# Kernel tuning notes

Hardware: AMD Instinct MI355X
Metric: run time of the kernel (lower is better)

Reference implementation:

```python
import jax, jax.numpy as jnp
import numpy as np

L, D, H, F = 6, 1024, 8, 2048
B, S, IN = 4, 2048, 128
DK = D // H
EPS = 1e-6


def layer_norm(x, s, b):
    mu = jnp.mean(x, -1, keepdims=True)
    var = jnp.mean((x - mu) ** 2, -1, keepdims=True)
    return (x - mu) * jax.lax.rsqrt(var + EPS) * s + b


def rotate_every_two(x):
    x1 = x[..., ::2]
    x2 = x[..., 1::2]
    return jnp.stack([-x2, x1], axis=-1).reshape(x.shape)


def rotary_tables():
    # torchscale RetNet xpos-style angles: each freq repeated twice (interleaved)
    angle = 1.0 / (10000.0 ** jnp.linspace(0.0, 1.0, DK // 2))
    angle = jnp.repeat(angle, 2)                      # [DK]
    idx = jnp.arange(S, dtype=jnp.float32)[:, None]   # [S,1]
    return jnp.sin(idx * angle), jnp.cos(idx * angle)  # [S,DK] each


def decay_mask():
    # gamma_h = 1 - 2^(-5-h); D[h,n,m] = gamma_h^(n-m) for n>=m else 0,
    # row-normalized by sqrt(row sum) as in torchscale.
    gamma = 1.0 - 2.0 ** (-5.0 - jnp.arange(H, dtype=jnp.float32))  # [H]
    n = jnp.arange(S)
    diff = jnp.clip(n[:, None] - n[None, :], 0)                      # [S,S]
    tril = n[:, None] >= n[None, :]
    m = jnp.where(tril[None], gamma[:, None, None] ** diff[None].astype(jnp.float32), 0.0)
    return m / jnp.sqrt(jnp.sum(m, -1, keepdims=True))               # [H,S,S]


def setup_inputs() -> dict:
    key = jax.random.key(0)
    ks = iter(jax.random.split(key, 24))
    p = lambda shape: jax.random.normal(next(ks), shape, jnp.float32) * 0.02
    return {
        "x": jax.random.normal(next(ks), (B, S, IN), jnp.float32),
        "W_in": p((IN, D)), "b_in": jnp.zeros((D,), jnp.float32),
        "Wq": p((L, D, D)), "Wk": p((L, D, D)), "Wv": p((L, D, D)),
        "Wg": p((L, D, D)), "Wo": p((L, D, D)),
        "gn_g": jnp.ones((L, D), jnp.float32),
        "ln1_s": jnp.ones((L, D), jnp.float32), "ln1_b": jnp.zeros((L, D), jnp.float32),
        "ffn_W1": p((L, D, F)), "ffn_b1": jnp.zeros((L, F), jnp.float32),
        "ffn_W2": p((L, F, D)), "ffn_b2": jnp.zeros((L, D), jnp.float32),
        "ln2_s": jnp.ones((L, D), jnp.float32), "ln2_b": jnp.zeros((L, D), jnp.float32),
        "lnf_s": jnp.ones((D,), jnp.float32), "lnf_b": jnp.zeros((D,), jnp.float32),
        "W_reg": p((D, 1)), "b_reg": jnp.zeros((1,), jnp.float32),
    }


def reference(x, W_in, b_in, Wq, Wk, Wv, Wg, Wo, gn_g, ln1_s, ln1_b,
              ffn_W1, ffn_b1, ffn_W2, ffn_b2, ln2_s, ln2_b, lnf_s, lnf_b,
              W_reg, b_reg):
    sin, cos = rotary_tables()
    dmask = decay_mask()  # [H,S,S]
    h = x @ W_in + b_in   # input_embed
    for l in range(L):
        # --- multi-scale retention (pre-norm) ---
        y = layer_norm(h, ln1_s[l], ln1_b[l])
        q = (y @ Wq[l]).reshape(B, S, H, DK).transpose(0, 2, 1, 3)
        k = (y @ Wk[l]).reshape(B, S, H, DK).transpose(0, 2, 1, 3) * (DK ** -0.5)
        v = (y @ Wv[l]).reshape(B, S, H, DK).transpose(0, 2, 1, 3)
        q = q * cos + rotate_every_two(q) * sin
        k = k * cos + rotate_every_two(k) * sin
        scores = jnp.einsum('bhnd,bhmd->bhnm', q, k)
        ret = scores * dmask[None]
        ret = ret / jnp.clip(jnp.abs(ret).sum(-1, keepdims=True), 1.0, None)
        o = jnp.einsum('bhnm,bhmd->bhnd', ret, v)
        # per-head group (RMS) norm
        o = o * jax.lax.rsqrt(jnp.mean(o * o, -1, keepdims=True) + EPS)
        o = o.transpose(0, 2, 1, 3).reshape(B, S, D) * gn_g[l]
        g = y @ Wg[l]
        h = h + (jax.nn.silu(g) * o) @ Wo[l]
        # --- FFN (pre-norm) ---
        y = layer_norm(h, ln2_s[l], ln2_b[l])
        h = h + jax.nn.gelu(y @ ffn_W1[l] + ffn_b1[l]) @ ffn_W2[l] + ffn_b2[l]
    h = layer_norm(h, lnf_s, lnf_b)
    out = 1.1 * jax.nn.sigmoid(h @ W_reg + b_reg) - 0.05
    return out.squeeze(-1)  # [B,S]
```

## Files before the change

### kernel.cpp

```cpp
#include <hip/hip_runtime.h>

#define L_ 6
#define D_ 1024
#define H_ 8
#define F_ 2048
#define B_ 4
#define S_ 2048
#define IN_ 128
#define DK_ 128
#define BS_ (B_*S_)
#define D2_ 4096

typedef short bf16x8 __attribute__((ext_vector_type(8)));
typedef float f32x4 __attribute__((ext_vector_type(4)));

__device__ inline float b2f(unsigned short u){ union{unsigned int i; float f;} v; v.i = ((unsigned int)u)<<16; return v.f; }
__device__ inline unsigned short f2b(float f){ union{unsigned int i; float f;} v; v.f = f; unsigned int r = v.i + 0x7FFFu + ((v.i>>16)&1u); return (unsigned short)(r>>16); }
__device__ inline unsigned int cvtpk(float lo, float hi){
    unsigned int r; asm("v_cvt_pk_bf16_f32 %0, %1, %2" : "=v"(r) : "v"(lo), "v"(hi)); return r;
}

__device__ inline void gld16(const void* g, void* l) {
    __builtin_amdgcn_global_load_lds((const __attribute__((address_space(1))) unsigned int*)g,
                                     (__attribute__((address_space(3))) unsigned int*)l, 16, 0, 0);
}

#define GBAR() do{ asm volatile("" ::: "memory"); __builtin_amdgcn_s_barrier(); asm volatile("" ::: "memory"); }while(0)

__global__ void f32_to_bf16_k(const float* __restrict__ in, unsigned short* __restrict__ out, int n)
{
    int i = blockIdx.x*256 + threadIdx.x;
    if (i < n) out[i] = f2b(in[i]);
}

__global__ void transpose_w_k(const float* __restrict__ in, unsigned short* __restrict__ out, int R, int C, size_t ostride)
{
    __shared__ float tile[32][33];
    int z = blockIdx.z;
    const float* pi = in + (size_t)z*R*C;
    unsigned short* po = out + (size_t)z*ostride;
    int c0 = blockIdx.x*32, r0 = blockIdx.y*32;
    int tx = threadIdx.x, ty = threadIdx.y;
    #pragma unroll
    for (int i=0;i<4;i++) tile[ty+i*8][tx] = pi[(size_t)(r0+ty+i*8)*C + c0+tx];
    __syncthreads();
    #pragma unroll
    for (int i=0;i<4;i++) po[(size_t)(c0+ty+i*8)*R + r0+tx] = f2b(tile[tx][ty+i*8]);
}

__global__ void transpose_v_k(const unsigned short* __restrict__ vb, unsigned short* __restrict__ vT)
{
    __shared__ unsigned short tile[32][33];
    int z = blockIdx.z;
    int b = z >> 3, hh = z & 7;
    int s0 = blockIdx.x*32, d0 = blockIdx.y*32;
    int tx = threadIdx.x, ty = threadIdx.y;
    #pragma unroll
    for (int i=0;i<4;i++) tile[ty+i*8][tx] = vb[(size_t)(b*S_ + s0+ty+i*8)*D2_ + hh*DK_ + d0+tx];
    __syncthreads();
    #pragma unroll
    for (int i=0;i<4;i++) vT[((size_t)z*DK_ + d0+ty+i*8)*S_ + s0+tx] = tile[tx][ty+i*8];
}

__global__ void build_sincos_k(float* __restrict__ cost, float* __restrict__ sint)
{
    int id = blockIdx.x*256 + threadIdx.x;
    int s = id >> 6, i = id & 63;
    float ang = powf(10000.f, -(float)i/63.f);
    float a = (float)s * ang;
    float sv = sinf(a), cv = cosf(a);
    sint[s*DK_ + 2*i] = sv; sint[s*DK_ + 2*i+1] = sv;
    cost[s*DK_ + 2*i] = cv; cost[s*DK_ + 2*i+1] = cv;
}

__global__ void build_dnorm_k(float* __restrict__ dnorm)
{
    int id = blockIdx.x*256 + threadIdx.x;
    int h = id >> 11, n = id & (S_-1);
    double g = 1.0 - exp2((double)(-5 - h));
    double sum = (1.0 - exp(((double)(n+1))*log(g))) / (1.0 - g);
    dnorm[id] = (float)(1.0/sqrt(sum));
}

__device__ inline float bsum(float v, float* red, int t)
{
    #pragma unroll
    for (int m=32; m; m>>=1) v += __shfl_xor(v, m);
    __syncthreads();
    if ((t & 63) == 0) red[t>>6] = v;
    __syncthreads();
    return red[0]+red[1]+red[2]+red[3];
}

__global__ __launch_bounds__(256) void ln_to_bf16_k(const float* __restrict__ x, const float* __restrict__ s,
                                                    const float* __restrict__ b, unsigned short* __restrict__ y)
{
    __shared__ float red[4];
    int row = blockIdx.x, t = threadIdx.x;
    const float* xr = x + (size_t)row * D_;
    float4 v = ((const float4*)xr)[t];
    float mu = bsum(v.x+v.y+v.z+v.w, red, t) * (1.f/D_);
    float d0=v.x-mu, d1=v.y-mu, d2=v.z-mu, d3=v.w-mu;
    float var = bsum(d0*d0+d1*d1+d2*d2+d3*d3, red, t) * (1.f/D_);
    float inv = rsqrtf(var + 1e-6f);
    int c = t*4;
    float o0 = d0*inv*s[c+0] + b[c+0];
    float o1 = d1*inv*s[c+1] + b[c+1];
    float o2 = d2*inv*s[c+2] + b[c+2];
    float o3 = d3*inv*s[c+3] + b[c+3];
    unsigned long long pk = (unsigned long long)f2b(o0) | ((unsigned long long)f2b(o1)<<16)
                          | ((unsigned long long)f2b(o2)<<32) | ((unsigned long long)f2b(o3)<<48);
    *(unsigned long long*)(y + (size_t)row*D_ + c) = pk;
}

template<int MODE, int BM, int BN, int WMC, int WNC>
__global__ __launch_bounds__(WMC*WNC*64, ((BM/WMC)*(BN/WNC) >= 128*64) ? 2 : 3)
void gemm4(const unsigned short* __restrict__ A,
           const unsigned short* __restrict__ Bt,
           const float* __restrict__ bias,
           void* __restrict__ Cv,
           int M, int N, int K)
{
    constexpr int THR = WMC*WNC*64;
    constexpr int IR  = BM/WMC/16;
    constexpr int JR  = BN/WNC/16;
    constexpr int ASZ = BM*64;
    constexpr int BSZ = BN*64;
    constexpr int RP  = THR/4;
    constexpr int AP  = BM/RP;
    constexpr int BP  = BN/RP;
    constexpr int Sa  = AP + BP;
    __shared__ unsigned char lds[2*(ASZ+BSZ)];

    const int tid = threadIdx.x, lane = tid & 63, w = tid >> 6;
    const int r16 = lane & 15, quad = (lane >> 4) & 3;
    const int wm = w / WNC, wn = w % WNC;

    const int nwg = (int)(gridDim.x * gridDim.y);
    int bid = (int)(blockIdx.y * gridDim.x + blockIdx.x);
    if ((nwg & 7) == 0) bid = (bid & 7) * (nwg >> 3) + (bid >> 3);
    const int m0 = (bid / (int)gridDim.x) * BM;
    const int n0 = (bid % (int)gridDim.x) * BN;

    const int srow = tid >> 2;
    const int schk = (tid & 3) ^ ((tid >> 3) & 3);
    const unsigned short* gA = A  + (size_t)(m0 + srow) * K + schk*8;
    const unsigned short* gB = Bt + (size_t)(n0 + srow) * K + schk*8;

    const int rchk = (quad ^ ((r16 >> 1) & 3)) * 16;
    const int aoff = (wm*(BM/WMC) + r16)*64 + rchk;
    const int boff = (wn*(BN/WNC) + r16)*64 + rchk;

    f32x4 acc[IR][JR];
    #pragma unroll
    for (int i=0;i<IR;i++)
      #pragma unroll
      for (int j=0;j<JR;j++) acc[i][j] = (f32x4){0.f,0.f,0.f,0.f};

    const int NT = K >> 5;

    auto stage = [&](int t){
        unsigned char* la = lds + (t&1)*(ASZ+BSZ);
        unsigned char* lb = la + ASZ;
        const size_t ko = (size_t)t * 32;
        #pragma unroll
        for (int p=0;p<AP;p++)
            gld16(gA + ko + (size_t)(p*RP)*K, la + p*RP*64 + tid*16);
        #pragma unroll
        for (int p=0;p<BP;p++)
            gld16(gB + ko + (size_t)(p*RP)*K, lb + p*RP*64 + tid*16);
    };

    auto compute = [&](int t){
        const unsigned char* ab = lds + (t&1)*(ASZ+BSZ);
        const unsigned char* bb = ab + ASZ;
        bf16x8 af[IR], bg[JR];
        #pragma unroll
        for (int i=0;i<IR;i++) af[i] = *(const bf16x8*)(ab + aoff + i*1024);
        #pragma unroll
        for (int j=0;j<JR;j++) bg[j] = *(const bf16x8*)(bb + boff + j*1024);
        __builtin_amdgcn_s_setprio(1);
        #pragma unroll
        for (int i=0;i<IR;i++)
          #pragma unroll
          for (int j=0;j<JR;j++)
            acc[i][j] = __builtin_amdgcn_mfma_f32_16x16x32_bf16(af[i], bg[j], acc[i][j], 0,0,0);
        __builtin_amdgcn_s_setprio(0);
    };

    stage(0);
    for (int t = 0; t < NT; ++t) {
        if (t + 1 < NT) {
            stage(t + 1);
            if constexpr (Sa == 4) asm volatile("s_waitcnt vmcnt(4)" ::: "memory");
            else                   asm volatile("s_waitcnt vmcnt(6)" ::: "memory");
        } else {
            asm volatile("s_waitcnt vmcnt(0)" ::: "memory");
        }
        GBAR();
        compute(t);
        GBAR();
    }

    float* Cf = (float*)Cv;
    unsigned short* Cb = (unsigned short*)Cv;
    #pragma unroll
    for (int j=0;j<JR;j++) {
      const int ccol = n0 + wn*(BN/WNC) + j*16 + r16;
      const float bv = bias ? bias[ccol] : 0.f;
      #pragma unroll
      for (int i=0;i<IR;i++) {
        #pragma unroll
        for (int r=0;r<4;r++) {
          const int crow = m0 + wm*(BM/WMC) + i*16 + quad*4 + r;
          float v = acc[i][j][r];
          if (MODE == 0) { Cf[(size_t)crow*N + ccol] = v + bv; }
          else if (MODE == 1) { Cf[(size_t)crow*N + ccol] += v + bv; }
          else if (MODE == 2) { Cb[(size_t)crow*N + ccol] = f2b(v); }
          else {
            v += bv;
            float t3 = tanhf(0.7978845608028654f*(v + 0.044715f*v*v*v));
            Cb[(size_t)crow*N + ccol] = f2b(0.5f*v*(1.f + t3));
          }
        }
      }
    }
}

__global__ __launch_bounds__(256) void rope_qk_k(unsigned short* __restrict__ qkvg,
                                                 const float* __restrict__ cost, const float* __restrict__ sint)
{
    int id = blockIdx.x*256 + threadIdx.x;
    int row = id >> 9;
    int d = (id & 511) * 2;
    int s = row & (S_-1);
    int dk = d & (DK_-1);
    float c0 = cost[s*DK_ + dk],   s0 = sint[s*DK_ + dk];
    float c1 = cost[s*DK_ + dk+1], s1 = sint[s*DK_ + dk+1];
    size_t off = (size_t)row*D2_ + d;
    unsigned int qu = *(unsigned int*)(qkvg + off);
    float q0 = b2f((unsigned short)(qu & 0xffffu)), q1 = b2f((unsigned short)(qu >> 16));
    float r0 = q0*c0 - q1*s0;
    float r1 = q1*c1 + q0*s1;
    *(unsigned int*)(qkvg + off) = (unsigned int)f2b(r0) | ((unsigned int)f2b(r1) << 16);
    const float sc = 0.08838834764831845f;
    unsigned int ku = *(unsigned int*)(qkvg + off + 1024);
    float k0 = b2f((unsigned short)(ku & 0xffffu))*sc, k1 = b2f((unsigned short)(ku >> 16))*sc;
    float t0 = k0*c0 - k1*s0;
    float t1 = k1*c1 + k0*s1;
    *(unsigned int*)(qkvg + off + 1024) = (unsigned int)f2b(t0) | ((unsigned int)f2b(t1) << 16);
}

__global__ __launch_bounds__(256, 2) void retention_k(const unsigned short* __restrict__ qk_base,
    const unsigned short* __restrict__ vT, const float* __restrict__ dnorm,
    const float* __restrict__ gng, unsigned short* __restrict__ attnin)
{
    __shared__ __align__(16) unsigned char lds[75776];
    const int pr = blockIdx.x;
    const int bh = blockIdx.y;
    const int b = bh >> 3, hh = bh & 7;
    const int tid = threadIdx.x, lane = tid & 63, w = tid >> 6;
    const int r16 = lane & 15, quad = lane >> 4;

    const float l2g = log2f(1.f - exp2f(-5.f - (float)hh));
    const int ithr = (int)(45.f / (-l2g));
    const unsigned int mkr = (r16 & 7) << 4;

    const int mk2  = ((tid >> 4) & 7) << 4;
    const int mkv2 = ((tid >> 3) & 7) << 4;
    const unsigned short* ksrc = qk_base + 1024 + ((size_t)(b*S_) + (tid>>4))*D2_ + hh*DK_
                                + ((((tid&15)*16) ^ mk2) >> 1);
    const unsigned short* vsrc = vT + ((size_t)bh*DK_ + (tid>>3))*S_ + ((((tid&7)*16) ^ mkv2) >> 1);

    float Aarr[4];
    #pragma unroll
    for (int r=0;r<4;r++) Aarr[r] = exp2f(l2g * (float)(63 - (w*16 + quad*4 + r)));

    float* dsums = (float*)(lds + 73728);
    float* ssums = (float*)(lds + 74752);

    auto stage = [&](int c2, int kt2){
        const unsigned short* s0 = ksrc + (size_t)kt2*64*D2_;
        #pragma unroll
        for (int i=0;i<4;i++)
            gld16(s0 + (size_t)i*16*D2_, lds + c2*16384 + i*4096 + w*1024);
        const unsigned short* s1 = vsrc + kt2*64;
        #pragma unroll
        for (int j=0;j<4;j++)
            gld16(s1 + (size_t)j*32*S_, lds + 32768 + c2*16384 + j*4096 + w*1024);
    };

    int cur = 0;

    #pragma unroll 1
    for (int seg = 0; seg < 2; ++seg) {
        const int qt = seg ? pr : (31 - pr);
        const int n0 = qt * 64;
        const int kt_start = max(0, (n0 - ithr) >> 6);

        bf16x8 qf[4][4];
        const unsigned short* qptr = qk_base + ((size_t)(b*S_ + n0 + r16))*D2_ + hh*DK_;
        #pragma unroll
        for (int qtl=0;qtl<4;qtl++)
          #pragma unroll
          for (int c=0;c<4;c++) qf[qtl][c] = *(const bf16x8*)(qptr + qtl*16*D2_ + c*32 + quad*8);

        f32x4 oacc[4][2];
        #pragma unroll
        for (int qtl=0;qtl<4;qtl++)
          #pragma unroll
          for (int dt=0;dt<2;dt++) oacc[qtl][dt] = (f32x4){0.f,0.f,0.f,0.f};
        float dsum[4] = {0.f,0.f,0.f,0.f};

        stage(cur, kt_start);

        #pragma unroll 1
        for (int kt = kt_start; kt <= qt; ++kt) {
            if (kt < qt) { stage(cur^1, kt+1); asm volatile("s_waitcnt vmcnt(8)" ::: "memory"); }
            else         { asm volatile("s_waitcnt vmcnt(0)" ::: "memory"); }
            GBAR();

            const unsigned char* kb = lds + cur*16384;
            bf16x8 kf[4];
            #pragma unroll
            for (int c=0;c<4;c++)
                kf[c] = *(const bf16x8*)(kb + (w*16 + r16)*256 + ((c*64 + quad*16) ^ mkr));
            f32x4 sf[4];
            #pragma unroll
            for (int qtl=0;qtl<4;qtl++) sf[qtl] = (f32x4){0.f,0.f,0.f,0.f};
            __builtin_amdgcn_s_setprio(1);
            #pragma unroll
            for (int c=0;c<4;c++)
              #pragma unroll
              for (int qtl=0;qtl<4;qtl++)
                sf[qtl] = __builtin_amdgcn_mfma_f32_16x16x32_bf16(kf[c], qf[qtl][c], sf[qtl], 0,0,0);
            __builtin_amdgcn_s_setprio(0);

            const bool diag = (kt == qt);
            #pragma unroll
            for (int qtl=0;qtl<4;qtl++) {
                float Bq = exp2f(l2g * (float)(n0 + qtl*16 + r16 - kt*64 - 63));
                float pv[4];
                #pragma unroll
                for (int r=0;r<4;r++) {
                    float p = sf[qtl][r] * Aarr[r] * Bq;
                    if (diag && (w*16 + quad*4 + r > qtl*16 + r16)) p = 0.f;
                    dsum[qtl] += fabsf(p);
                    pv[r] = p;
                }
                unsigned long long pk = (unsigned long long)cvtpk(pv[0], pv[1])
                                      | ((unsigned long long)cvtpk(pv[2], pv[3]) << 32);
                *(unsigned long long*)(lds + 65536 + (qtl*16 + r16)*128 + ((w*32 + quad*8) ^ mkr)) = pk;
            }
            asm volatile("s_waitcnt lgkmcnt(0)" ::: "memory");
            GBAR();

            const unsigned char* vb = lds + 32768 + cur*16384;
            bf16x8 pa[4][2], vf[2][2];
            #pragma unroll
            for (int qtl=0;qtl<4;qtl++)
              #pragma unroll
              for (int ks=0;ks<2;ks++)
                pa[qtl][ks] = *(const bf16x8*)(lds + 65536 + (qtl*16 + r16)*128 + ((ks*64 + quad*16) ^ mkr));
            #pragma unroll
            for (int dt=0;dt<2;dt++)
              #pragma unroll
              for (int ks=0;ks<2;ks++)
                vf[dt][ks] = *(const bf16x8*)(vb + (w*32 + dt*16 + r16)*128 + ((ks*64 + quad*16) ^ mkr));
            __builtin_amdgcn_s_setprio(1);
            #pragma unroll
            for (int qtl=0;qtl<4;qtl++)
              #pragma unroll
              for (int dt=0;dt<2;dt++)
                #pragma unroll
                for (int ks=0;ks<2;ks++)
                  oacc[qtl][dt] = __builtin_amdgcn_mfma_f32_16x16x32_bf16(pa[qtl][ks], vf[dt][ks], oacc[qtl][dt], 0,0,0);
            __builtin_amdgcn_s_setprio(0);
            GBAR();
            cur ^= 1;
        }

        #pragma unroll
        for (int qtl=0;qtl<4;qtl++) {
            float dv = dsum[qtl];
            dv += __shfl_xor(dv, 16); dv += __shfl_xor(dv, 32);
            if (lane < 16) dsums[w*64 + qtl*16 + r16] = dv;
        }
        __syncthreads();
        float scl[4][4], pss[4][4];
        #pragma unroll
        for (int qtl=0;qtl<4;qtl++) {
            #pragma unroll
            for (int r=0;r<4;r++) {
                int nl = qtl*16 + quad*4 + r;
                float dv = dsums[nl] + dsums[64+nl] + dsums[128+nl] + dsums[192+nl];
                float nr = dnorm[hh*S_ + n0 + nl];
                float sc = nr / fmaxf(1.f, dv * nr);
                scl[qtl][r] = sc;
                float s2 = 0.f;
                #pragma unroll
                for (int dt=0;dt<2;dt++) { float t = oacc[qtl][dt][r]*sc; s2 += t*t; }
                s2 += __shfl_xor(s2,1); s2 += __shfl_xor(s2,2);
                s2 += __shfl_xor(s2,4); s2 += __shfl_xor(s2,8);
                pss[qtl][r] = s2;
            }
        }
        if (r16 == 0) {
            #pragma unroll
            for (int qtl=0;qtl<4;qtl++)
              #pragma unroll
              for (int r=0;r<4;r++)
                ssums[w*64 + qtl*16 + quad*4 + r] = pss[qtl][r];
        }
        __syncthreads();
        #pragma unroll
        for (int qtl=0;qtl<4;qtl++) {
            float rms[4];
            #pragma unroll
            for (int r=0;r<4;r++) {
                int nl = qtl*16 + quad*4 + r;
                float s2 = ssums[nl] + ssums[64+nl] + ssums[128+nl] + ssums[192+nl];
                rms[r] = rsqrtf(s2*(1.f/DK_) + 1e-6f);
            }
            #pragma unroll
            for (int dt=0;dt<2;dt++) {
                int d = w*32 + dt*16 + r16;
                float gg = gng[hh*DK_ + d];
                #pragma unroll
                for (int r=0;r<4;r++) {
                    int n = n0 + qtl*16 + quad*4 + r;
                    float gv = b2f(qk_base[(size_t)(b*S_ + n)*D2_ + 3072 + hh*DK_ + d]);
                    float sg = gv / (1.f + expf(-gv));
                    float ov = oacc[qtl][dt][r]*scl[qtl][r]*rms[r]*gg;
                    attnin[(size_t)(b*S_ + n)*D_ + hh*DK_ + d] = f2b(ov*sg);
                }
            }
        }
        __syncthreads();
    }
}

__global__ __launch_bounds__(256) void head_out_k(const float* __restrict__ h, const float* __restrict__ s,
    const float* __restrict__ b, const float* __restrict__ wreg, const float* __restrict__ breg,
    float* __restrict__ out)
{
    __shared__ float red[4];
    int row = blockIdx.x, t = threadIdx.x;
    const float* xr = h + (size_t)row*D_;
    float4 v = ((const float4*)xr)[t];
    float mu = bsum(v.x+v.y+v.z+v.w, red, t) * (1.f/D_);
    float d0=v.x-mu, d1=v.y-mu, d2=v.z-mu, d3=v.w-mu;
    float var = bsum(d0*d0+d1*d1+d2*d2+d3*d3, red, t) * (1.f/D_);
    float inv = rsqrtf(var + 1e-6f);
    int c = t*4;
    float dot = (d0*inv*s[c+0]+b[c+0])*wreg[c+0] + (d1*inv*s[c+1]+b[c+1])*wreg[c+1]
              + (d2*inv*s[c+2]+b[c+2])*wreg[c+2] + (d3*inv*s[c+3]+b[c+3])*wreg[c+3];
    dot = bsum(dot, red, t);
    if (t == 0) out[row] = 1.1f / (1.f + expf(-(dot + breg[0]))) - 0.05f;
}

extern "C" void kernel_launch(void* const* d_in, const int* in_sizes, int n_in,
                              void* d_out, int out_size, void* d_ws, size_t ws_size,
                              hipStream_t stream)
{
    (void)in_sizes; (void)n_in; (void)out_size; (void)ws_size;
    const float* x    = (const float*)d_in[0];
    const float* W_in = (const float*)d_in[1];
    const float* b_in = (const float*)d_in[2];
    const float* Wq   = (const float*)d_in[3];
    const float* Wk   = (const float*)d_in[4];
    const float* Wv   = (const float*)d_in[5];
    const float* Wg   = (const float*)d_in[6];
    const float* Wo   = (const float*)d_in[7];
    const float* gn_g = (const float*)d_in[8];
    const float* ln1s = (const float*)d_in[9];
    const float* ln1b = (const float*)d_in[10];
    const float* W1   = (const float*)d_in[11];
    const float* b1   = (const float*)d_in[12];
    const float* W2   = (const float*)d_in[13];
    const float* b2   = (const float*)d_in[14];
    const float* ln2s = (const float*)d_in[15];
    const float* ln2b = (const float*)d_in[16];
    const float* lnfs = (const float*)d_in[17];
    const float* lnfb = (const float*)d_in[18];
    const float* Wreg = (const float*)d_in[19];
    const float* breg = (const float*)d_in[20];

    char* ws = (char*)d_ws;
    size_t off = 0;
    auto alloc = [&](size_t bytes) { char* p = ws + off; off += (bytes + 255) & ~(size_t)255; return p; };

    const size_t DD = (size_t)D_*D_;
    unsigned short* wqkvgT = (unsigned short*)alloc((size_t)L_*4*DD*2);
    unsigned short* woT  = (unsigned short*)alloc((size_t)L_*DD*2);
    unsigned short* w1T  = (unsigned short*)alloc((size_t)L_*D_*F_*2);
    unsigned short* w2T  = (unsigned short*)alloc((size_t)L_*D_*F_*2);
    unsigned short* winT = (unsigned short*)alloc((size_t)D_*IN_*2);
    unsigned short* x_bf = (unsigned short*)alloc((size_t)BS_*IN_*2);
    float*          hbuf = (float*)alloc((size_t)BS_*D_*4);
    unsigned short* y_bf = (unsigned short*)alloc((size_t)BS_*D_*2);
    unsigned short* qkvg = (unsigned short*)alloc((size_t)BS_*D2_*2);
    unsigned short* vTb  = (unsigned short*)alloc((size_t)BS_*D_*2);
    float*          cost = (float*)alloc((size_t)S_*DK_*4);
    float*          sint = (float*)alloc((size_t)S_*DK_*4);
    float*          dnrm = (float*)alloc((size_t)H_*S_*4);
    unsigned short* attn = y_bf;
    unsigned short* midb = qkvg;

    dim3 tb(32, 8);

    f32_to_bf16_k<<<(BS_*IN_)/256, 256, 0, stream>>>(x, x_bf, BS_*IN_);
    transpose_w_k<<<dim3(32,32,L_), tb, 0, stream>>>(Wq, wqkvgT + 0*DD, D_, D_, 4*DD);
    transpose_w_k<<<dim3(32,32,L_), tb, 0, stream>>>(Wk, wqkvgT + 1*DD, D_, D_, 4*DD);
    transpose_w_k<<<dim3(32,32,L_), tb, 0, stream>>>(Wv, wqkvgT + 2*DD, D_, D_, 4*DD);
    transpose_w_k<<<dim3(32,32,L_), tb, 0, stream>>>(Wg, wqkvgT + 3*DD, D_, D_, 4*DD);
    transpose_w_k<<<dim3(32,32,L_), tb, 0, stream>>>(Wo, woT, D_, D_, DD);
    transpose_w_k<<<dim3(64,32,L_), tb, 0, stream>>>(W1, w1T, D_, F_, (size_t)D_*F_);
    transpose_w_k<<<dim3(32,64,L_), tb, 0, stream>>>(W2, w2T, F_, D_, (size_t)D_*F_);
    transpose_w_k<<<dim3(32, 4, 1), tb, 0, stream>>>(W_in, winT, IN_, D_, (size_t)D_*IN_);
    build_sincos_k<<<(S_*64)/256, 256, 0, stream>>>(cost, sint);
    build_dnorm_k<<<(H_*S_)/256, 256, 0, stream>>>(dnrm);

    gemm4<0,128,128,2,2><<<dim3(D_/128, BS_/128), 256, 0, stream>>>(x_bf, winT, b_in, hbuf, BS_, D_, IN_);

    for (int l = 0; l < L_; ++l) {
        ln_to_bf16_k<<<BS_, 256, 0, stream>>>(hbuf, ln1s + l*D_, ln1b + l*D_, y_bf);
        gemm4<2,256,256,2,4><<<dim3(D2_/256, BS_/256), 512, 0, stream>>>(y_bf, wqkvgT + (size_t)l*4*DD, nullptr, qkvg, BS_, D2_, D_);
        rope_qk_k<<<(BS_*D_/2)/256, 256, 0, stream>>>(qkvg, cost, sint);
        transpose_v_k<<<dim3(S_/32, DK_/32, B_*H_), tb, 0, stream>>>(qkvg + 2048, vTb);
        retention_k<<<dim3(16, B_*H_), 256, 0, stream>>>(qkvg, vTb, dnrm, gn_g + l*D_, attn);
        gemm4<1,128,128,2,2><<<dim3(D_/128, BS_/128), 256, 0, stream>>>(attn, woT + (size_t)l*DD, nullptr, hbuf, BS_, D_, D_);
        ln_to_bf16_k<<<BS_, 256, 0, stream>>>(hbuf, ln2s + l*D_, ln2b + l*D_, y_bf);
        gemm4<3,256,128,2,2><<<dim3(F_/128, BS_/256), 256, 0, stream>>>(y_bf, w1T + (size_t)l*D_*F_, b1 + l*F_, midb, BS_, F_, D_);
        gemm4<1,128,128,2,2><<<dim3(D_/128, BS_/128), 256, 0, stream>>>(midb, w2T + (size_t)l*D_*F_, b2 + l*D_, hbuf, BS_, D_, F_);
    }

    head_out_k<<<BS_, 256, 0, stream>>>(hbuf, lnfs, lnfb, Wreg, breg, (float*)d_out);
}
```

Measured before the change: 2.144 ms.

## Replace GEMM with triple-buffered split-phase kernel using 256-wide N tiles

The templated GEMM becomes a fixed 512-thread, 8-wave kernel with BN=256 and BM of 128 or 256. Shared memory goes from double to triple buffering, with two K-steps prefetched ahead. Each K-step is split into two halves that interleave A and B stage loads with MFMA work. All projection and FFN GEMMs move to this kernel, so the Wo/W2/input GEMMs now use larger 128x256 tiles. The aim is to hide global-load latency and raise MFMA utilisation, at the cost of more LDS and barriers, fewer workgroups for the N=1024 GEMMs, and lower occupancy.

```diff
diff --git a/kernel.cpp b/kernel.cpp
--- a/kernel.cpp
+++ b/kernel.cpp
@@ -113,28 +113,27 @@
     *(unsigned long long*)(y + (size_t)row*D_ + c) = pk;
 }
 
-template<int MODE, int BM, int BN, int WMC, int WNC>
-__global__ __launch_bounds__(WMC*WNC*64, ((BM/WMC)*(BN/WNC) >= 128*64) ? 2 : 3)
-void gemm4(const unsigned short* __restrict__ A,
+template<int MODE, int BM>
+__global__ __launch_bounds__(512, (BM == 256) ? 2 : 4)
+void gemm5(const unsigned short* __restrict__ A,
            const unsigned short* __restrict__ Bt,
            const float* __restrict__ bias,
            void* __restrict__ Cv,
            int M, int N, int K)
 {
-    constexpr int THR = WMC*WNC*64;
-    constexpr int IR  = BM/WMC/16;
-    constexpr int JR  = BN/WNC/16;
+    constexpr int BN  = 256;
+    constexpr int IR  = BM/2/16;
+    constexpr int JR  = 4;
     constexpr int ASZ = BM*64;
     constexpr int BSZ = BN*64;
-    constexpr int RP  = THR/4;
-    constexpr int AP  = BM/RP;
-    constexpr int BP  = BN/RP;
+    constexpr int AP  = BM/128;
+    constexpr int BP  = 2;
     constexpr int Sa  = AP + BP;
-    __shared__ unsigned char lds[2*(ASZ+BSZ)];
+    __shared__ unsigned char lds[3*(ASZ+BSZ)];
 
     const int tid = threadIdx.x, lane = tid & 63, w = tid >> 6;
     const int r16 = lane & 15, quad = (lane >> 4) & 3;
-    const int wm = w / WNC, wn = w % WNC;
+    const int wm = w >> 2, wn = w & 3;
 
     const int nwg = (int)(gridDim.x * gridDim.y);
     int bid = (int)(blockIdx.y * gridDim.x + blockIdx.x);
@@ -148,8 +147,8 @@
     const unsigned short* gB = Bt + (size_t)(n0 + srow) * K + schk*8;
 
     const int rchk = (quad ^ ((r16 >> 1) & 3)) * 16;
-    const int aoff = (wm*(BM/WMC) + r16)*64 + rchk;
-    const int boff = (wn*(BN/WNC) + r16)*64 + rchk;
+    const int aoff = (wm*(BM/2) + r16)*64 + rchk;
+    const int boff = (wn*64 + r16)*64 + rchk;
 
     f32x4 acc[IR][JR];
     #pragma unroll
@@ -159,60 +158,85 @@
 
     const int NT = K >> 5;
 
-    auto stage = [&](int t){
-        unsigned char* la = lds + (t&1)*(ASZ+BSZ);
-        unsigned char* lb = la + ASZ;
+    auto stageA = [&](int t, int slot){
+        unsigned char* la = lds + slot*(ASZ+BSZ);
         const size_t ko = (size_t)t * 32;
         #pragma unroll
         for (int p=0;p<AP;p++)
-            gld16(gA + ko + (size_t)(p*RP)*K, la + p*RP*64 + tid*16);
+            gld16(gA + ko + (size_t)(p*128)*K, la + p*8192 + tid*16);
+    };
+    auto stageB = [&](int t, int slot){
+        unsigned char* lb = lds + slot*(ASZ+BSZ) + ASZ;
+        const size_t ko = (size_t)t * 32;
         #pragma unroll
         for (int p=0;p<BP;p++)
-            gld16(gB + ko + (size_t)(p*RP)*K, lb + p*RP*64 + tid*16);
+            gld16(gB + ko + (size_t)(p*128)*K, lb + p*8192 + tid*16);
     };
 
-    auto compute = [&](int t){
-        const unsigned char* ab = lds + (t&1)*(ASZ+BSZ);
+    stageA(0, 0); stageB(0, 0);
+    stageA(1, 1); stageB(1, 1);
+    if constexpr (Sa == 4) asm volatile("s_waitcnt vmcnt(4)" ::: "memory");
+    else                   asm volatile("s_waitcnt vmcnt(3)" ::: "memory");
+    GBAR();
+
+    int st = 0;
+    for (int t = 0; t < NT; ++t) {
+        const unsigned char* ab = lds + st*(ASZ+BSZ);
         const unsigned char* bb = ab + ASZ;
+        int s2 = st + 2; if (s2 >= 3) s2 -= 3;
+        const bool pre = (t + 2 < NT);
+
         bf16x8 af[IR], bg[JR];
         #pragma unroll
-        for (int i=0;i<IR;i++) af[i] = *(const bf16x8*)(ab + aoff + i*1024);
-        #pragma unroll
-        for (int j=0;j<JR;j++) bg[j] = *(const bf16x8*)(bb + boff + j*1024);
+        for (int i=0;i<IR/2;i++) af[i] = *(const bf16x8*)(ab + aoff + i*1024);
+        #pragma unroll
+        for (int j=0;j<JR;j++)   bg[j] = *(const bf16x8*)(bb + boff + j*1024);
+        if (pre) stageA(t+2, s2);
+        GBAR();
+        asm volatile("s_waitcnt lgkmcnt(0)" ::: "memory");
         __builtin_amdgcn_s_setprio(1);
         #pragma unroll
-        for (int i=0;i<IR;i++)
+        for (int i=0;i<IR/2;i++)
           #pragma unroll
           for (int j=0;j<JR;j++)
             acc[i][j] = __builtin_amdgcn_mfma_f32_16x16x32_bf16(af[i], bg[j], acc[i][j], 0,0,0);
         __builtin_amdgcn_s_setprio(0);
-    };
-
-    stage(0);
-    for (int t = 0; t < NT; ++t) {
-        if (t + 1 < NT) {
-            stage(t + 1);
+        GBAR();
+
+        #pragma unroll
+        for (int i=IR/2;i<IR;i++) af[i] = *(const bf16x8*)(ab + aoff + i*1024);
+        if (pre) {
+            stageB(t+2, s2);
             if constexpr (Sa == 4) asm volatile("s_waitcnt vmcnt(4)" ::: "memory");
-            else                   asm volatile("s_waitcnt vmcnt(6)" ::: "memory");
-        } else {
+            else                   asm volatile("s_waitcnt vmcnt(3)" ::: "memory");
+        } else if (t + 1 < NT) {
             asm volatile("s_waitcnt vmcnt(0)" ::: "memory");
         }
         GBAR();
-        compute(t);
+        asm volatile("s_waitcnt lgkmcnt(0)" ::: "memory");
+        __builtin_amdgcn_s_setprio(1);
+        #pragma unroll
+        for (int i=IR/2;i<IR;i++)
+          #pragma unroll
+          for (int j=0;j<JR;j++)
+            acc[i][j] = __builtin_amdgcn_mfma_f32_16x16x32_bf16(af[i], bg[j], acc[i][j], 0,0,0);
+        __builtin_amdgcn_s_setprio(0);
         GBAR();
+
+        st = (st + 1 == 3) ? 0 : st + 1;
     }
 
     float* Cf = (float*)Cv;
     unsigned short* Cb = (unsigned short*)Cv;
     #pragma unroll
     for (int j=0;j<JR;j++) {
-      const int ccol = n0 + wn*(BN/WNC) + j*16 + r16;
+      const int ccol = n0 + wn*64 + j*16 + r16;
       const float bv = bias ? bias[ccol] : 0.f;
       #pragma unroll
       for (int i=0;i<IR;i++) {
         #pragma unroll
         for (int r=0;r<4;r++) {
-          const int crow = m0 + wm*(BM/WMC) + i*16 + quad*4 + r;
+          const int crow = m0 + wm*(BM/2) + i*16 + quad*4 + r;
           float v = acc[i][j][r];
           if (MODE == 0) { Cf[(size_t)crow*N + ccol] = v + bv; }
           else if (MODE == 1) { Cf[(size_t)crow*N + ccol] += v + bv; }
@@ -521,18 +545,18 @@
     build_sincos_k<<<(S_*64)/256, 256, 0, stream>>>(cost, sint);
     build_dnorm_k<<<(H_*S_)/256, 256, 0, stream>>>(dnrm);
 
-    gemm4<0,128,128,2,2><<<dim3(D_/128, BS_/128), 256, 0, stream>>>(x_bf, winT, b_in, hbuf, BS_, D_, IN_);
+    gemm5<0,128><<<dim3(D_/256, BS_/128), 512, 0, stream>>>(x_bf, winT, b_in, hbuf, BS_, D_, IN_);
 
     for (int l = 0; l < L_; ++l) {
         ln_to_bf16_k<<<BS_, 256, 0, stream>>>(hbuf, ln1s + l*D_, ln1b + l*D_, y_bf);
-        gemm4<2,256,256,2,4><<<dim3(D2_/256, BS_/256), 512, 0, stream>>>(y_bf, wqkvgT + (size_t)l*4*DD, nullptr, qkvg, BS_, D2_, D_);
+        gemm5<2,256><<<dim3(D2_/256, BS_/256), 512, 0, stream>>>(y_bf, wqkvgT + (size_t)l*4*DD, nullptr, qkvg, BS_, D2_, D_);
         rope_qk_k<<<(BS_*D_/2)/256, 256, 0, stream>>>(qkvg, cost, sint);
         transpose_v_k<<<dim3(S_/32, DK_/32, B_*H_), tb, 0, stream>>>(qkvg + 2048, vTb);
         retention_k<<<dim3(16, B_*H_), 256, 0, stream>>>(qkvg, vTb, dnrm, gn_g + l*D_, attn);
-        gemm4<1,128,128,2,2><<<dim3(D_/128, BS_/128), 256, 0, stream>>>(attn, woT + (size_t)l*DD, nullptr, hbuf, BS_, D_, D_);
+        gemm5<1,128><<<dim3(D_/256, BS_/128), 512, 0, stream>>>(attn, woT + (size_t)l*DD, nullptr, hbuf, BS_, D_, D_);
         ln_to_bf16_k<<<BS_, 256, 0, stream>>>(hbuf, ln2s + l*D_, ln2b + l*D_, y_bf);
-        gemm4<3,256,128,2,2><<<dim3(F_/128, BS_/256), 256, 0, stream>>>(y_bf, w1T + (size_t)l*D_*F_, b1 + l*F_, midb, BS_, F_, D_);
-        gemm4<1,128,128,2,2><<<dim3(D_/128, BS_/128), 256, 0, stream>>>(midb, w2T + (size_t)l*D_*F_, b2 + l*D_, hbuf, BS_, D_, F_);
+        gemm5<3,256><<<dim3(F_/256, BS_/256), 512, 0, stream>>>(y_bf, w1T + (size_t)l*D_*F_, b1 + l*F_, midb, BS_, F_, D_);
+        gemm5<1,128><<<dim3(D_/256, BS_/128), 512, 0, stream>>>(midb, w2T + (size_t)l*D_*F_, b2 + l*D_, hbuf, BS_, D_, F_);
     }
 
     head_out_k<<<BS_, 256, 0, stream>>>(hbuf, lnfs, lnfb, Wreg, breg, (float*)d_out);
```

Measured after the change: 2.132 ms. Within noise of the previous version (-0.5%).
